# Performance work log

Hardware: AMD Instinct MI355X
Metric: run time of the kernel (lower is better)

## Reference

```python
import jax, jax.numpy as jnp
import numpy as np

N, E = 50000, 800000
IN, HID, OUT, HEADS = 256, 128, 256, 4
CAT = HEADS * HID  # 512


def _gat(x, ei_src, ei_dst, W, a_src, a_dst, b, heads, out_ch, concat):
    """PyG-style GATConv with self-loops. x:[N,F]; returns [N,heads*out_ch] or [N,out_ch]."""
    n = x.shape[0]
    loop = jnp.arange(n, dtype=ei_src.dtype)
    src = jnp.concatenate([ei_src, loop])
    dst = jnp.concatenate([ei_dst, loop])
    h = (x @ W).reshape(n, heads, out_ch)              # [N,H,C]
    al_s = jnp.einsum('nhc,hc->nh', h, a_src)          # [N,H]
    al_d = jnp.einsum('nhc,hc->nh', h, a_dst)
    e = jax.nn.leaky_relu(al_s[src] + al_d[dst], 0.2)  # [E',H]
    emax = jax.ops.segment_max(e, dst, num_segments=n)
    ee = jnp.exp(e - emax[dst])
    denom = jax.ops.segment_sum(ee, dst, num_segments=n)
    alpha = ee / (denom[dst] + 1e-16)                  # segment softmax over incoming edges
    out = jax.ops.segment_sum(h[src] * alpha[:, :, None], dst, num_segments=n)  # [N,H,C]
    out = out.reshape(n, heads * out_ch) if concat else out.mean(axis=1)
    return out + b


def setup_inputs() -> dict:
    key = jax.random.key(0)
    ks = jax.random.split(key, 20)
    g = lambda k, shape, fan: (jax.random.normal(k, shape, jnp.float32) / np.sqrt(fan)).astype(jnp.float32)
    return {
        'x': jax.random.normal(ks[0], (N, IN), jnp.float32),
        'edge_index': jax.random.randint(ks[1], (2, E), 0, N, dtype=jnp.int32),
        # GAT layer 1: IN -> HID x 4 heads, concat
        'W1': g(ks[2], (IN, CAT), IN), 'a_src1': g(ks[3], (HEADS, HID), HID),
        'a_dst1': g(ks[4], (HEADS, HID), HID), 'b1': jnp.zeros((CAT,), jnp.float32),
        # GAT layer 2: CAT -> HID x 4 heads, concat
        'W2': g(ks[5], (CAT, CAT), CAT), 'a_src2': g(ks[6], (HEADS, HID), HID),
        'a_dst2': g(ks[7], (HEADS, HID), HID), 'b2': jnp.zeros((CAT,), jnp.float32),
        # GAT layer 3: CAT -> OUT, 1 head, no concat
        'W3': g(ks[8], (CAT, OUT), CAT), 'a_src3': g(ks[9], (1, OUT), OUT),
        'a_dst3': g(ks[10], (1, OUT), OUT), 'b3': jnp.zeros((OUT,), jnp.float32),
        # response_generator MLP: OUT -> 2*HID -> HID -> OUT
        'M1': g(ks[11], (OUT, 2 * HID), OUT), 'mb1': jnp.zeros((2 * HID,), jnp.float32),
        'M2': g(ks[12], (2 * HID, HID), 2 * HID), 'mb2': jnp.zeros((HID,), jnp.float32),
        'M3': g(ks[13], (HID, OUT), HID), 'mb3': jnp.zeros((OUT,), jnp.float32),
    }


def reference(x, edge_index, W1, a_src1, a_dst1, b1, W2, a_src2, a_dst2, b2,
              W3, a_src3, a_dst3, b3, M1, mb1, M2, mb2, M3, mb3):
    src, dst = edge_index[0], edge_index[1]
    h = _gat(x, src, dst, W1, a_src1, a_dst1, b1, HEADS, HID, True)
    h = jax.nn.elu(h)  # dropout is identity in eval mode
    h = _gat(h, src, dst, W2, a_src2, a_dst2, b2, HEADS, HID, True)
    h = jax.nn.elu(h)
    h = _gat(h, src, dst, W3, a_src3, a_dst3, b3, 1, OUT, False)
    # response generator MLP (dropout identity in eval)
    r = jax.nn.relu(h @ M1 + mb1)
    r = jax.nn.relu(r @ M2 + mb2)
    return r @ M3 + mb3
```

## Files before the change

kernel.cpp:

```cpp
#include <hip/hip_runtime.h>
#include <cstdint>
#include <cstddef>

#define HEADS  4
#define HIDC   128
#define CATF   512
#define IN_F   256
#define OUT_F  256

typedef _Float16 f16x8 __attribute__((ext_vector_type(8)));
typedef _Float16 f16x4 __attribute__((ext_vector_type(4)));
typedef float f32x4  __attribute__((ext_vector_type(4)));

__device__ __forceinline__ void async16(const void* g, void* l) {
    __builtin_amdgcn_global_load_lds((const __attribute__((address_space(1))) void*)g,
                                     (__attribute__((address_space(3))) void*)l, 16, 0, 0);
}

__global__ void init_counts(int* cnt, int N) {
    int i = blockIdx.x * blockDim.x + threadIdx.x;
    if (i < N) cnt[i] = 1;
}

__global__ void count_dst(const int* __restrict__ dst, int E, int* cnt) {
    int i = blockIdx.x * blockDim.x + threadIdx.x;
    if (i < E) atomicAdd(&cnt[dst[i]], 1);
}

__global__ void scan_partial(const int* __restrict__ cnt, int* excl, int* bsum, int N) {
    __shared__ int tmp[256];
    int i = blockIdx.x * 256 + threadIdx.x;
    int v = (i < N) ? cnt[i] : 0;
    tmp[threadIdx.x] = v;
    __syncthreads();
    for (int off = 1; off < 256; off <<= 1) {
        int t = ((int)threadIdx.x >= off) ? tmp[threadIdx.x - off] : 0;
        __syncthreads();
        tmp[threadIdx.x] += t;
        __syncthreads();
    }
    if (i < N) excl[i] = tmp[threadIdx.x] - v;
    if (threadIdx.x == 255) bsum[blockIdx.x] = tmp[255];
}

__global__ void scan_bsums(int* bsum, int nb) {
    __shared__ int tmp[256];
    int v = ((int)threadIdx.x < nb) ? bsum[threadIdx.x] : 0;
    tmp[threadIdx.x] = v;
    __syncthreads();
    for (int off = 1; off < 256; off <<= 1) {
        int t = ((int)threadIdx.x >= off) ? tmp[threadIdx.x - off] : 0;
        __syncthreads();
        tmp[threadIdx.x] += t;
        __syncthreads();
    }
    if ((int)threadIdx.x < nb) bsum[threadIdx.x] = tmp[threadIdx.x] - v;
}

__global__ void add_carry(int* indptr, int* pos, const int* __restrict__ bsum, int N, int total) {
    int i = blockIdx.x * blockDim.x + threadIdx.x;
    if (i < N) {
        int v = indptr[i] + bsum[i >> 8];
        indptr[i] = v;
        pos[i] = v;
    }
    if (i == 0) indptr[N] = total;
}

__global__ void scatter_edges(const int* __restrict__ src, const int* __restrict__ dst,
                              int E, int N, int* pos, int* esrc) {
    int i = blockIdx.x * blockDim.x + threadIdx.x;
    int total = E + N;
    if (i >= total) return;
    int s, d;
    if (i < E) { s = src[i]; d = dst[i]; }
    else       { s = i - E;  d = s; }
    int p = atomicAdd(&pos[d], 1);
    esrc[p] = s;
}

__global__ void conv_h16(const float* __restrict__ in, _Float16* __restrict__ out, long n4) {
    long i = (long)blockIdx.x * blockDim.x + threadIdx.x;
    if (i >= n4) return;
    float4 v = ((const float4*)in)[i];
    f16x4 o = { (_Float16)v.x, (_Float16)v.y, (_Float16)v.z, (_Float16)v.w };
    ((f16x4*)out)[i] = o;
}

struct WDesc { const float* W; _Float16* hi; _Float16* lo; int K; int N; int off; };
struct WPack { WDesc d[6]; int total; };
__global__ void conv_w_all(WPack p) {
    int idx = blockIdx.x * blockDim.x + threadIdx.x;
    if (idx >= p.total) return;
    int wi = 0;
    while (wi < 5 && idx >= p.d[wi + 1].off) wi++;
    const WDesc& w = p.d[wi];
    int li = idx - w.off;
    int n = li / w.K, k = li - n * w.K;
    float v = w.W[(size_t)k * w.N + n];
    _Float16 h = (_Float16)v;
    w.hi[(size_t)n * w.K + k] = h;
    if (w.lo) w.lo[(size_t)n * w.K + k] = (_Float16)(v - (float)h);
}

__global__ void zero2(float* a, float* b, int n) {
    int i = blockIdx.x * blockDim.x + threadIdx.x;
    if (i < n) { a[i] = 0.f; b[i] = 0.f; }
}

#define TM 128
#define TN 128
#define TK 32
template <int MODE, int NMF, int ATTN>
__global__ __launch_bounds__(256) void gemm_bt(
        const _Float16* __restrict__ A,
        const _Float16* __restrict__ Bh, const _Float16* __restrict__ Bl,
        const float* __restrict__ bias,
        float* __restrict__ out_f, _Float16* __restrict__ out_h16,
        const float* __restrict__ asrc, const float* __restrict__ adst,
        float* __restrict__ al_s, float* __restrict__ al_d,
        int M, int N, int K, int act) {
    __shared__ __align__(16) _Float16 sA[TM * TK], sBh[TN * TK];
    __shared__ __align__(16) _Float16 sBl[NMF == 2 ? TN * TK : 16];
    __shared__ float sred[ATTN ? TM * 4 : 4];
    int tid = threadIdx.x;
    int wave = tid >> 6, lane = tid & 63;
    int m0 = blockIdx.y * TM, n0 = blockIdx.x * TN;
    int wm = wave >> 1, wn = wave & 1;
    int srow = lane >> 2;
    int skel = (lane & 3) * 8;
    int fr = lane & 15, quad = lane >> 4;

    f32x4 acc[4][4];
#pragma unroll
    for (int i = 0; i < 4; i++)
#pragma unroll
        for (int j = 0; j < 4; j++) acc[i][j] = (f32x4){0.f, 0.f, 0.f, 0.f};

    for (int k0 = 0; k0 < K; k0 += TK) {
        __syncthreads();
#pragma unroll
        for (int c = 0; c < 2; c++) {
            int chunk = wave * 2 + c;
            int r = chunk * 16 + srow;
            int gmA = m0 + r; if (gmA >= M) gmA = M - 1;
            int gnB = n0 + r;
            size_t aoff = (size_t)gmA * K + k0 + skel;
            size_t boff = (size_t)gnB * K + k0 + skel;
            int ldso = chunk * 512;
            async16(A + aoff, &sA[ldso]);
            async16(Bh + boff, &sBh[ldso]);
            if (NMF == 2) async16(Bl + boff, &sBl[ldso]);
        }
        __syncthreads();

        f16x8 fa[4], fbh[4], fbl[4];
#pragma unroll
        for (int i = 0; i < 4; i++) {
            int ra = (wm * 64 + i * 16 + fr) * TK + quad * 8;
            int rb = (wn * 64 + i * 16 + fr) * TK + quad * 8;
            fa[i]  = *(const f16x8*)&sA[ra];
            fbh[i] = *(const f16x8*)&sBh[rb];
            if (NMF == 2) fbl[i] = *(const f16x8*)&sBl[rb];
        }
#pragma unroll
        for (int i = 0; i < 4; i++)
#pragma unroll
            for (int j = 0; j < 4; j++) {
                if (NMF == 2)
                    acc[i][j] = __builtin_amdgcn_mfma_f32_16x16x32_f16(fa[i], fbl[j], acc[i][j], 0, 0, 0);
                acc[i][j] = __builtin_amdgcn_mfma_f32_16x16x32_f16(fa[i], fbh[j], acc[i][j], 0, 0, 0);
            }
    }

    float avs[4], avd[4];
    if (ATTN) {
#pragma unroll
        for (int j = 0; j < 4; j++) {
            int gn = n0 + wn * 64 + j * 16 + fr;
            avs[j] = asrc[gn];
            avd[j] = adst[gn];
        }
        __syncthreads();
    }

#pragma unroll
    for (int i = 0; i < 4; i++)
#pragma unroll
        for (int r = 0; r < 4; r++) {
            int gm = m0 + wm * 64 + i * 16 + quad * 4 + r;
            if (gm >= M) continue;
            float ps = 0.f, pd = 0.f;
#pragma unroll
            for (int j = 0; j < 4; j++) {
                int gn = n0 + wn * 64 + j * 16 + fr;
                float v = acc[i][j][r];
                if (bias) v += bias[gn];
                if (act == 1) v = fmaxf(v, 0.f);
                size_t o = (size_t)gm * N + gn;
                if (MODE == 1) out_f[o] = v;
                else           out_h16[o] = (_Float16)v;
                if (ATTN) { ps += v * avs[j]; pd += v * avd[j]; }
            }
            if (ATTN) {
#pragma unroll
                for (int off = 1; off < 16; off <<= 1) {
                    ps += __shfl_xor(ps, off);
                    pd += __shfl_xor(pd, off);
                }
                if (fr == 0) {
                    int lrow = wm * 64 + i * 16 + quad * 4 + r;
                    sred[lrow * 4 + 0 * 2 + wn] = ps;
                    sred[lrow * 4 + 1 * 2 + wn] = pd;
                }
            }
        }

    if (ATTN) {
        __syncthreads();
        if (tid < TM) {
            int gm = m0 + tid;
            if (gm < M) {
                float s = sred[tid * 4 + 0] + sred[tid * 4 + 1];
                float d = sred[tid * 4 + 2] + sred[tid * 4 + 3];
                if (ATTN == 1) {
                    int head = n0 >> 7;
                    al_s[gm * HEADS + head] = s;
                    al_d[gm * HEADS + head] = d;
                } else {
                    atomicAdd(&al_s[gm], s);
                    atomicAdd(&al_d[gm], d);
                }
            }
        }
    }
}

template <int CT, int H>
__global__ void gat_aggregate_f(const _Float16* __restrict__ h,
                                const float* __restrict__ al_s, const float* __restrict__ al_d,
                                const int* __restrict__ indptr, const int* __restrict__ esrc,
                                const float* __restrict__ bias,
                                _Float16* __restrict__ oh,
                                int N, int act) {
    typedef _Float16 hvec __attribute__((ext_vector_type(CT)));
    const int C_ALL = CT * 64;
    int n = (blockIdx.x * blockDim.x + threadIdx.x) >> 6;
    int lane = threadIdx.x & 63;
    if (n >= N) return;
    int head = (lane * H) >> 6;
    float ald = al_d[n * H + head];
    float acc[CT];
#pragma unroll
    for (int k = 0; k < CT; k++) acc[k] = 0.f;
    float dsum = 0.f;

    int beg = indptr[n], end = indptr[n + 1];
    int idx = beg;
    for (; idx + 8 <= end; idx += 8) {
        int s[8]; float av[8]; hvec v[8];
#pragma unroll
        for (int u = 0; u < 8; u++) s[u] = esrc[idx + u];
#pragma unroll
        for (int u = 0; u < 8; u++) av[u] = al_s[s[u] * H + head];
#pragma unroll
        for (int u = 0; u < 8; u++) v[u] = *(const hvec*)(h + (size_t)s[u] * C_ALL + lane * CT);
#pragma unroll
        for (int u = 0; u < 8; u++) {
            float e = av[u] + ald;
            e = e > 0.f ? e : 0.2f * e;
            e = fminf(e, 60.f);
            float w = __expf(e);
            dsum += w;
#pragma unroll
            for (int k = 0; k < CT; k++) acc[k] += w * (float)v[u][k];
        }
    }
    if (idx + 4 <= end) {
        int s[4]; float av[4]; hvec v[4];
#pragma unroll
        for (int u = 0; u < 4; u++) s[u] = esrc[idx + u];
#pragma unroll
        for (int u = 0; u < 4; u++) av[u] = al_s[s[u] * H + head];
#pragma unroll
        for (int u = 0; u < 4; u++) v[u] = *(const hvec*)(h + (size_t)s[u] * C_ALL + lane * CT);
#pragma unroll
        for (int u = 0; u < 4; u++) {
            float e = av[u] + ald;
            e = e > 0.f ? e : 0.2f * e;
            e = fminf(e, 60.f);
            float w = __expf(e);
            dsum += w;
#pragma unroll
            for (int k = 0; k < CT; k++) acc[k] += w * (float)v[u][k];
        }
        idx += 4;
    }
    for (; idx < end; idx++) {
        int s0 = esrc[idx];
        float e = al_s[s0 * H + head] + ald;
        e = e > 0.f ? e : 0.2f * e;
        e = fminf(e, 60.f);
        float w = __expf(e);
        dsum += w;
        hvec v0 = *(const hvec*)(h + (size_t)s0 * C_ALL + lane * CT);
#pragma unroll
        for (int k = 0; k < CT; k++) acc[k] += w * (float)v0[k];
    }

    float inv = 1.f / (dsum + 1e-16f);
    size_t ob = (size_t)n * C_ALL + lane * CT;
    const float* bp = bias + lane * CT;
    hvec o;
#pragma unroll
    for (int k = 0; k < CT; k++) {
        float v = acc[k] * inv + bp[k];
        if (act == 1) v = v > 0.f ? v : (__expf(v) - 1.f);
        o[k] = (_Float16)v;
    }
    __builtin_nontemporal_store(o, (hvec*)(oh + ob));
}

extern "C" void kernel_launch(void* const* d_in, const int* in_sizes, int n_in,
                              void* d_out, int out_size, void* d_ws, size_t ws_size,
                              hipStream_t stream) {
    const float* x   = (const float*)d_in[0];
    const int*   ei  = (const int*)d_in[1];
    const float* W1  = (const float*)d_in[2];
    const float* as1 = (const float*)d_in[3];
    const float* ad1 = (const float*)d_in[4];
    const float* b1  = (const float*)d_in[5];
    const float* W2  = (const float*)d_in[6];
    const float* as2 = (const float*)d_in[7];
    const float* ad2 = (const float*)d_in[8];
    const float* b2  = (const float*)d_in[9];
    const float* W3  = (const float*)d_in[10];
    const float* as3 = (const float*)d_in[11];
    const float* ad3 = (const float*)d_in[12];
    const float* b3  = (const float*)d_in[13];
    const float* M1  = (const float*)d_in[14];
    const float* mb1 = (const float*)d_in[15];
    const float* M2  = (const float*)d_in[16];
    const float* mb2 = (const float*)d_in[17];
    const float* M3  = (const float*)d_in[18];
    const float* mb3 = (const float*)d_in[19];
    float* out = (float*)d_out;

    const int N = in_sizes[0] / IN_F;
    const int E = in_sizes[1] / 2;
    const int* src = ei;
    const int* dst = ei + E;

    char* ws = (char*)d_ws;
    auto alloc = [&](size_t bytes) { char* p = ws; ws += (bytes + 255) & ~(size_t)255; return p; };
    _Float16* H16 = (_Float16*)alloc((size_t)N * CATF * 2);
    _Float16* P16 = (_Float16*)alloc((size_t)N * CATF * 2);
    float* al_s = (float*)alloc((size_t)N * HEADS * 4);
    float* al_d = (float*)alloc((size_t)N * HEADS * 4);
    int* cnt    = (int*)alloc((size_t)N * 4);
    int* pos    = (int*)alloc((size_t)N * 4);
    int* indptr = (int*)alloc((size_t)(N + 1) * 4);
    int* esrc   = (int*)alloc((size_t)(E + N) * 4);
    int* bsum   = (int*)alloc(256 * 4);
    auto walloc = [&](int k, int n, _Float16*& h, _Float16*& l, bool need_lo) {
        h = (_Float16*)alloc((size_t)k * n * 2);
        l = need_lo ? (_Float16*)alloc((size_t)k * n * 2) : nullptr;
    };
    _Float16 *W1h, *W1l, *W2h, *W2l, *W3h, *W3l, *M1h, *M1l, *M2h, *M2l, *M3h, *M3l;
    walloc(IN_F, CATF, W1h, W1l, false);
    walloc(CATF, CATF, W2h, W2l, false);
    walloc(CATF, OUT_F, W3h, W3l, false);
    walloc(OUT_F, 2 * HIDC, M1h, M1l, true);
    walloc(2 * HIDC, HIDC, M2h, M2l, true);
    walloc(HIDC, OUT_F, M3h, M3l, true);

    const int nb = (N + 255) / 256;
    init_counts<<<(N + 255) / 256, 256, 0, stream>>>(cnt, N);
    count_dst<<<(E + 255) / 256, 256, 0, stream>>>(dst, E, cnt);
    scan_partial<<<nb, 256, 0, stream>>>(cnt, indptr, bsum, N);
    scan_bsums<<<1, 256, 0, stream>>>(bsum, nb);
    add_carry<<<nb, 256, 0, stream>>>(indptr, pos, bsum, N, E + N);
    scatter_edges<<<(E + N + 255) / 256, 256, 0, stream>>>(src, dst, E, N, pos, esrc);

    {
        WPack p;
        int off = 0;
        auto setd = [&](int i, const float* W, _Float16* h, _Float16* l, int K, int Nc) {
            p.d[i] = WDesc{W, h, l, K, Nc, off};
            off += K * Nc;
        };
        setd(0, W1, W1h, W1l, IN_F, CATF);
        setd(1, W2, W2h, W2l, CATF, CATF);
        setd(2, W3, W3h, W3l, CATF, OUT_F);
        setd(3, M1, M1h, M1l, OUT_F, 2 * HIDC);
        setd(4, M2, M2h, M2l, 2 * HIDC, HIDC);
        setd(5, M3, M3h, M3l, HIDC, OUT_F);
        p.total = off;
        conv_w_all<<<(off + 255) / 256, 256, 0, stream>>>(p);
    }

    auto gemm_gat = [&](const _Float16* Ap, const _Float16* Bhp, _Float16* oh,
                        const float* asrc, const float* adst, int M_, int Nc, int K, int attn_mode) {
        dim3 grid(Nc / TN, (M_ + TM - 1) / TM);
        if (attn_mode == 1)
            gemm_bt<2, 1, 1><<<grid, 256, 0, stream>>>(Ap, Bhp, nullptr, nullptr, nullptr, oh,
                                                       asrc, adst, al_s, al_d, M_, Nc, K, 0);
        else
            gemm_bt<2, 1, 2><<<grid, 256, 0, stream>>>(Ap, Bhp, nullptr, nullptr, nullptr, oh,
                                                       asrc, adst, al_s, al_d, M_, Nc, K, 0);
    };
    auto gemm_mlp16 = [&](const _Float16* Ap, const _Float16* Bhp, const _Float16* Blp,
                          const float* bias, _Float16* oh, int M_, int Nc, int K, int act) {
        dim3 grid(Nc / TN, (M_ + TM - 1) / TM);
        gemm_bt<2, 2, 0><<<grid, 256, 0, stream>>>(Ap, Bhp, Blp, bias, nullptr, oh,
                                                   nullptr, nullptr, nullptr, nullptr, M_, Nc, K, act);
    };

    const int gwav = (N + 3) / 4;

    conv_h16<<<((long)N * IN_F / 4 + 255) / 256, 256, 0, stream>>>(x, P16, (long)N * IN_F / 4);

    gemm_gat(P16, W1h, H16, as1, ad1, N, CATF, IN_F, 1);
    gat_aggregate_f<8, HEADS><<<gwav, 256, 0, stream>>>(H16, al_s, al_d, indptr, esrc,
                                                        b1, P16, N, 1);
    gemm_gat(P16, W2h, H16, as2, ad2, N, CATF, CATF, 1);
    gat_aggregate_f<8, HEADS><<<gwav, 256, 0, stream>>>(H16, al_s, al_d, indptr, esrc,
                                                        b2, P16, N, 1);
    zero2<<<(N + 255) / 256, 256, 0, stream>>>(al_s, al_d, N);
    gemm_gat(P16, W3h, H16, as3, ad3, N, OUT_F, CATF, 2);
    gat_aggregate_f<4, 1><<<gwav, 256, 0, stream>>>(H16, al_s, al_d, indptr, esrc,
                                                    b3, P16, N, 0);
    _Float16* Q16 = H16;
    _Float16* R16 = P16 + (size_t)N * OUT_F;
    gemm_mlp16(P16, M1h, M1l, mb1, Q16, N, 2 * HIDC, OUT_F, 1);
    gemm_mlp16(Q16, M2h, M2l, mb2, R16, N, HIDC, 2 * HIDC, 1);
    {
        dim3 grid(OUT_F / TN, (N + TM - 1) / TM);
        gemm_bt<1, 2, 0><<<grid, 256, 0, stream>>>(R16, M3h, M3l, mb3, out, nullptr,
                                                   nullptr, nullptr, nullptr, nullptr,
                                                   N, OUT_F, HIDC, 0);
    }
}
```

Measured before the change: 828.5 us.

## Double-buffer LDS tiles in GEMM to overlap global loads with MFMA

The GEMM main loop now uses two LDS buffers per operand, issuing the async global-to-LDS loads for the next K-step before computing on the current one. Manual vmcnt waits and raw s_barrier calls replace the two __syncthreads per iteration, so memory latency can overlap with MFMA work. LDS usage doubles, which may lower occupancy. The hand-counted vmcnt values depend on exactly how many loads are in flight, and the __syncthreads before the attention epilogue was removed.

```diff
diff --git a/kernel.cpp b/kernel.cpp
--- a/kernel.cpp
+++ b/kernel.cpp
@@ -120,8 +120,8 @@
         const float* __restrict__ asrc, const float* __restrict__ adst,
         float* __restrict__ al_s, float* __restrict__ al_d,
         int M, int N, int K, int act) {
-    __shared__ __align__(16) _Float16 sA[TM * TK], sBh[TN * TK];
-    __shared__ __align__(16) _Float16 sBl[NMF == 2 ? TN * TK : 16];
+    __shared__ __align__(16) _Float16 sA[2][TM * TK], sBh[2][TN * TK];
+    __shared__ __align__(16) _Float16 sBl[NMF == 2 ? 2 * TN * TK : 16];
     __shared__ float sred[ATTN ? TM * 4 : 4];
     int tid = threadIdx.x;
     int wave = tid >> 6, lane = tid & 63;
@@ -137,8 +137,7 @@
 #pragma unroll
         for (int j = 0; j < 4; j++) acc[i][j] = (f32x4){0.f, 0.f, 0.f, 0.f};
 
-    for (int k0 = 0; k0 < K; k0 += TK) {
-        __syncthreads();
+    auto stage = [&](int buf, int k0) {
 #pragma unroll
         for (int c = 0; c < 2; c++) {
             int chunk = wave * 2 + c;
@@ -148,20 +147,34 @@
             size_t aoff = (size_t)gmA * K + k0 + skel;
             size_t boff = (size_t)gnB * K + k0 + skel;
             int ldso = chunk * 512;
-            async16(A + aoff, &sA[ldso]);
-            async16(Bh + boff, &sBh[ldso]);
-            if (NMF == 2) async16(Bl + boff, &sBl[ldso]);
-        }
-        __syncthreads();
+            async16(A + aoff, &sA[buf][ldso]);
+            async16(Bh + boff, &sBh[buf][ldso]);
+            if (NMF == 2) async16(Bl + boff, &sBl[buf * (TN * TK) + ldso]);
+        }
+    };
+
+    const int nsteps = K / TK;
+    stage(0, 0);
+    int cur = 0;
+    for (int s = 0; s < nsteps; ++s, cur ^= 1) {
+        if (s + 1 < nsteps) {
+            stage(cur ^ 1, (s + 1) * TK);
+            if (NMF == 2) asm volatile("s_waitcnt vmcnt(6)" ::: "memory");
+            else          asm volatile("s_waitcnt vmcnt(4)" ::: "memory");
+        } else {
+            asm volatile("s_waitcnt vmcnt(0)" ::: "memory");
+        }
+        __builtin_amdgcn_s_barrier();
+        __builtin_amdgcn_sched_barrier(0);
 
         f16x8 fa[4], fbh[4], fbl[4];
 #pragma unroll
         for (int i = 0; i < 4; i++) {
             int ra = (wm * 64 + i * 16 + fr) * TK + quad * 8;
             int rb = (wn * 64 + i * 16 + fr) * TK + quad * 8;
-            fa[i]  = *(const f16x8*)&sA[ra];
-            fbh[i] = *(const f16x8*)&sBh[rb];
-            if (NMF == 2) fbl[i] = *(const f16x8*)&sBl[rb];
+            fa[i]  = *(const f16x8*)&sA[cur][ra];
+            fbh[i] = *(const f16x8*)&sBh[cur][rb];
+            if (NMF == 2) fbl[i] = *(const f16x8*)&sBl[cur * (TN * TK) + rb];
         }
 #pragma unroll
         for (int i = 0; i < 4; i++)
@@ -171,6 +184,8 @@
                     acc[i][j] = __builtin_amdgcn_mfma_f32_16x16x32_f16(fa[i], fbl[j], acc[i][j], 0, 0, 0);
                 acc[i][j] = __builtin_amdgcn_mfma_f32_16x16x32_f16(fa[i], fbh[j], acc[i][j], 0, 0, 0);
             }
+        __builtin_amdgcn_sched_barrier(0);
+        __builtin_amdgcn_s_barrier();
     }
 
     float avs[4], avd[4];
@@ -181,7 +196,6 @@
             avs[j] = asrc[gn];
             avd[j] = adst[gn];
         }
-        __syncthreads();
     }
 
 #pragma unroll
```

After: 823.4 us. Within noise of the previous version (-0.6%).
